# Optimization experiments

Measured on AMD Instinct MI355X. Metric: run time of the kernel, lower is better.

Reference implementation:

```python
import jax, jax.numpy as jnp
import numpy as np

K0 = 0.7978845608028654  # sqrt(2/pi)
C1 = 0.044715

def _gelu_tanh(x):
    # tanh-approx GELU, matching the Triton kernel's math
    return 0.5 * x * (1.0 + jnp.tanh(K0 * (x + C1 * x * x * x)))

def setup_inputs() -> dict:
    key = jax.random.key(0)
    k1, k2, k3 = jax.random.split(key, 3)
    B, C_in, H, W = 32, 64, 128, 128
    C_out, KH = 128, 3
    x = jax.random.normal(k1, (B, C_in, H, W), dtype=jnp.float32)
    weight = jax.random.normal(k2, (C_out, C_in, KH, KH), dtype=jnp.float32)
    bias = jax.random.normal(k3, (C_out,), dtype=jnp.float32)
    return {"x": x, "weight": weight, "bias": bias}

def reference(x, weight, bias):
    # Valid conv2d, stride 1 (NCHW, OIHW)
    y = jax.lax.conv_general_dilated(
        x, weight,
        window_strides=(1, 1), padding="VALID",
        dimension_numbers=("NCHW", "OIHW", "NCHW"))
    y = y + bias[None, :, None, None]
    y = _gelu_tanh(y)
    # global average pool over spatial dims -> [B, C_out]
    return jnp.mean(y, axis=(2, 3))
```

## Files before the change

kernel.cpp:

```cpp
#include <hip/hip_runtime.h>
#include <cstdint>
#include <cstddef>

#define GK0 0.7978845608028654f
#define GC1 0.044715f

typedef __attribute__((ext_vector_type(8))) short short8;
typedef __attribute__((ext_vector_type(4))) float floatx4;

__device__ __forceinline__ unsigned short f2bf(float f) {
  union { float f; unsigned int u; } v; v.f = f;
  unsigned int r = v.u + 0x7fffu + ((v.u >> 16) & 1u);
  return (unsigned short)(r >> 16);
}

__device__ __forceinline__ void gl_lds16(const unsigned short* g, unsigned short* l) {
  __builtin_amdgcn_global_load_lds(
      (const __attribute__((address_space(1))) unsigned int*)g,
      (__attribute__((address_space(3))) unsigned int*)l, 16, 0, 0);
}

__global__ void k_wt(const float* __restrict__ w, unsigned short* __restrict__ wt,
                     float* __restrict__ out) {
  if (blockIdx.x == 0) {
    for (int i = threadIdx.x; i < 32 * 128; i += 256) out[i] = 0.0f;
  }
  int t = blockIdx.x * 256 + threadIdx.x;
  if (t >= 128 * 64 * 9) return;
  int co = t / 576; int r = t - co * 576; int ci = r / 9; int khw = r - ci * 9;
  wt[(khw * 128 + co) * 64 + ci] = f2bf(w[t]);
}

__global__ __launch_bounds__(256, 2) void k_conv(
    const float* __restrict__ x, const unsigned short* __restrict__ wt,
    const float* __restrict__ bias, float* __restrict__ out) {
  __shared__ __align__(16) unsigned short Bs[4 * 72 * 64];
  __shared__ __align__(16) unsigned short As[4][4096];
  const int tid = threadIdx.x, lane = tid & 63, wv = tid >> 6;
  const int w0 = blockIdx.x * 64, h0 = blockIdx.y * 2, b = blockIdx.z;
  const int wm = wv & 1, wn = wv >> 1;
  const int m = lane & 15, q = lane >> 4;
  unsigned short* Asw = As[wv];

  const int srcswz = (lane >> 3) * 64 + (((lane & 7) ^ (lane >> 3)) << 3);
  auto stageA = [&](int khw) {
    const unsigned short* src = wt + khw * 8192 + wm * 4096 + srcswz;
#pragma unroll
    for (int c = 0; c < 8; c++) gl_lds16(src + c * 512, Asw + c * 512);
  };

  floatx4 acc[4][4];
#pragma unroll
  for (int i = 0; i < 4; i++)
#pragma unroll
    for (int j = 0; j < 4; j++) acc[i][j] = (floatx4){0.f, 0.f, 0.f, 0.f};

  stageA(0);

  const float* xb0 = x + (size_t)b * 64 * 16384 + (size_t)h0 * 128;
#pragma unroll
  for (int t3 = 0; t3 < 3; t3++) {
    float4 u[6];
#pragma unroll
    for (int j = 0; j < 6; j++) {
      const int v = (t3 * 6 + j) * 256 + tid;
      const int r = v / 1152, rem = v - r * 1152;
      const int ci = rem / 18, i = rem - ci * 18;
      const int wc = min(w0 + 4 * i, 124);
      u[j] = *(const float4*)(xb0 + (size_t)ci * 16384 + r * 128 + wc);
    }
#pragma unroll
    for (int j = 0; j < 6; j++) {
      const int v = (t3 * 6 + j) * 256 + tid;
      const int r = v / 1152, rem = v - r * 1152;
      const int ci = rem / 18, i = rem - ci * 18;
      unsigned short* brow = Bs + r * 4608;
      union { float4 v4; float f[4]; } w4; w4.v4 = u[j];
#pragma unroll
      for (int k2 = 0; k2 < 4; k2++) {
        const int p = 4 * i + k2;
        brow[p * 64 + (ci ^ ((p & 7) << 3))] = f2bf(w4.f[k2]);
      }
    }
  }
  __syncthreads();
#pragma unroll
  for (int kh = 0; kh < 3; kh++)
#pragma unroll
    for (int kw = 0; kw < 3; kw++) {
      const int khw = kh * 3 + kw;
      const unsigned short* bcur = Bs + (wn + kh) * 4608;
      short8 a[2][4], bf[2][4];
#pragma unroll
      for (int half = 0; half < 2; half++) {
        const int colb = half * 32 + q * 8;
#pragma unroll
        for (int mt = 0; mt < 4; mt++)
          a[half][mt] =
              *(const short8*)(Asw + (mt * 16 + m) * 64 + (colb ^ ((m & 7) << 3)));
#pragma unroll
        for (int nt = 0; nt < 4; nt++)
          bf[half][nt] = *(const short8*)(bcur + (nt * 16 + m + kw) * 64 +
                                          (colb ^ (((m + kw) & 7) << 3)));
      }
      asm volatile("s_waitcnt lgkmcnt(0)" ::: "memory");
      if (khw < 8) stageA(khw + 1);
#pragma unroll
      for (int half = 0; half < 2; half++)
#pragma unroll
        for (int mt = 0; mt < 4; mt++)
#pragma unroll
          for (int nt = 0; nt < 4; nt++)
            acc[mt][nt] = __builtin_amdgcn_mfma_f32_16x16x32_bf16(
                a[half][mt], bf[half][nt], acc[mt][nt], 0, 0, 0);
      if (khw < 8)
        asm volatile("s_waitcnt vmcnt(0)" ::: "memory");
    }

  const float inv_area = 1.0f / (126.0f * 126.0f);
  float* orow = out + b * 128;
#pragma unroll
  for (int mt = 0; mt < 4; mt++)
#pragma unroll
    for (int r2 = 0; r2 < 4; r2++) {
      const int co = wm * 64 + mt * 16 + q * 4 + r2;
      const float bv = bias[co];
      float s = 0.f;
#pragma unroll
      for (int nt = 0; nt < 4; nt++) {
        float y = acc[mt][nt][r2] + bv;
        float u = GK0 * (y + GC1 * y * y * y);
        float e = __expf(-2.0f * u);
        float g = y * __builtin_amdgcn_rcpf(1.0f + e);
        if (w0 + nt * 16 + m < 126) s += g;
      }
#pragma unroll
      for (int d = 1; d < 16; d <<= 1) s += __shfl_xor(s, d, 64);
      if (m == 0) atomicAdd(&orow[co], s * inv_area);
    }
}

extern "C" void kernel_launch(void* const* d_in, const int* in_sizes, int n_in,
                              void* d_out, int out_size, void* d_ws, size_t ws_size,
                              hipStream_t stream) {
  const float* x    = (const float*)d_in[0];
  const float* w    = (const float*)d_in[1];
  const float* bias = (const float*)d_in[2];
  float* out = (float*)d_out;

  unsigned short* wbuf = (unsigned short*)d_ws;
  if (ws_size < (size_t)9 * 128 * 64 * 2 + 4096) return;

  k_wt<<<288, 256, 0, stream>>>(w, wbuf, out);
  k_conv<<<dim3(2, 63, 32), 256, 0, stream>>>(x, wbuf, bias, out);
}
```

Before: 369.4 us.

## Make conv blocks persistent over row pairs with rolling input ring buffer

Each block now processes up to 8 output row pairs instead of one, keeping a 4-row circular LDS buffer of bf16 input rows and prefetching the next two rows into registers during the MFMA loop. Weight tiles are restaged cyclically per tap, and GELU pooling is accumulated in registers per row pair, so there are fewer atomics and input rows are reused between adjacent pairs. The grid shrinks from 63 to 8 row groups, which cuts launch parallelism to 512 blocks and adds extra syncs and register pressure from the prefetch buffers.

```diff
diff --git a/kernel.cpp b/kernel.cpp
--- a/kernel.cpp
+++ b/kernel.cpp
@@ -34,10 +34,11 @@
 __global__ __launch_bounds__(256, 2) void k_conv(
     const float* __restrict__ x, const unsigned short* __restrict__ wt,
     const float* __restrict__ bias, float* __restrict__ out) {
-  __shared__ __align__(16) unsigned short Bs[4 * 72 * 64];
+  __shared__ __align__(16) unsigned short Bs[4][4608];
   __shared__ __align__(16) unsigned short As[4][4096];
   const int tid = threadIdx.x, lane = tid & 63, wv = tid >> 6;
-  const int w0 = blockIdx.x * 64, h0 = blockIdx.y * 2, b = blockIdx.z;
+  const int w0 = blockIdx.x * 64, g = blockIdx.y, b = blockIdx.z;
+  const int npair = (g < 7) ? 8 : 7;
   const int wm = wv & 1, wn = wv >> 1;
   const int m = lane & 15, q = lane >> 4;
   unsigned short* Asw = As[wv];
@@ -49,73 +50,143 @@
     for (int c = 0; c < 8; c++) gl_lds16(src + c * 512, Asw + c * 512);
   };
 
+  const float* xg = x + (size_t)b * 64 * 16384 + (size_t)(16 * g) * 128;
+
+  float bvv[4][4];
+#pragma unroll
+  for (int mt = 0; mt < 4; mt++)
+#pragma unroll
+    for (int r2 = 0; r2 < 4; r2++)
+      bvv[mt][r2] = bias[wm * 64 + mt * 16 + q * 4 + r2];
+
   floatx4 acc[4][4];
+  float pool[4][4];
 #pragma unroll
   for (int i = 0; i < 4; i++)
 #pragma unroll
-    for (int j = 0; j < 4; j++) acc[i][j] = (floatx4){0.f, 0.f, 0.f, 0.f};
+    for (int j = 0; j < 4; j++) {
+      acc[i][j] = (floatx4){0.f, 0.f, 0.f, 0.f};
+      pool[i][j] = 0.f;
+    }
 
   stageA(0);
 
-  const float* xb0 = x + (size_t)b * 64 * 16384 + (size_t)h0 * 128;
 #pragma unroll
   for (int t3 = 0; t3 < 3; t3++) {
-    float4 u[6];
+    float4 u6[6];
 #pragma unroll
     for (int j = 0; j < 6; j++) {
-      const int v = (t3 * 6 + j) * 256 + tid;
-      const int r = v / 1152, rem = v - r * 1152;
-      const int ci = rem / 18, i = rem - ci * 18;
-      const int wc = min(w0 + 4 * i, 124);
-      u[j] = *(const float4*)(xb0 + (size_t)ci * 16384 + r * 128 + wc);
+      const int u = (t3 * 6 + j) * 256 + tid;
+      const int r = u / 1152, rem = u - r * 1152;
+      const int ci = rem / 18, ch = rem - ci * 18;
+      u6[j] = *(const float4*)(xg + (size_t)ci * 16384 + r * 128 + min(w0 + 4 * ch, 124));
     }
 #pragma unroll
     for (int j = 0; j < 6; j++) {
-      const int v = (t3 * 6 + j) * 256 + tid;
-      const int r = v / 1152, rem = v - r * 1152;
-      const int ci = rem / 18, i = rem - ci * 18;
-      unsigned short* brow = Bs + r * 4608;
-      union { float4 v4; float f[4]; } w4; w4.v4 = u[j];
-#pragma unroll
-      for (int k2 = 0; k2 < 4; k2++) {
-        const int p = 4 * i + k2;
-        brow[p * 64 + (ci ^ ((p & 7) << 3))] = f2bf(w4.f[k2]);
+      const int u = (t3 * 6 + j) * 256 + tid;
+      const int r = u / 1152, rem = u - r * 1152;
+      const int ci = rem / 18, ch = rem - ci * 18;
+      union { float4 v4; float f[4]; } fu; fu.v4 = u6[j];
+#pragma unroll
+      for (int e = 0; e < 4; e++) {
+        const int p = 4 * ch + e;
+        Bs[r][p * 64 + (ci ^ ((p & 7) << 3))] = f2bf(fu.f[e]);
       }
     }
   }
   __syncthreads();
-#pragma unroll
-  for (int kh = 0; kh < 3; kh++)
-#pragma unroll
-    for (int kw = 0; kw < 3; kw++) {
-      const int khw = kh * 3 + kw;
-      const unsigned short* bcur = Bs + (wn + kh) * 4608;
-      short8 a[2][4], bf[2][4];
-#pragma unroll
-      for (int half = 0; half < 2; half++) {
-        const int colb = half * 32 + q * 8;
-#pragma unroll
-        for (int mt = 0; mt < 4; mt++)
-          a[half][mt] =
-              *(const short8*)(Asw + (mt * 16 + m) * 64 + (colb ^ ((m & 7) << 3)));
-#pragma unroll
-        for (int nt = 0; nt < 4; nt++)
-          bf[half][nt] = *(const short8*)(bcur + (nt * 16 + m + kw) * 64 +
-                                          (colb ^ (((m + kw) & 7) << 3)));
-      }
-      asm volatile("s_waitcnt lgkmcnt(0)" ::: "memory");
-      if (khw < 8) stageA(khw + 1);
-#pragma unroll
-      for (int half = 0; half < 2; half++)
-#pragma unroll
-        for (int mt = 0; mt < 4; mt++)
+
+  for (int hp = 0; hp < npair; hp++) {
+    const int more = (hp + 1 < npair);
+    float4 ru[9];
+    unsigned int pk[9][2];
+#pragma unroll
+    for (int kh = 0; kh < 3; kh++) {
+#pragma unroll
+      for (int kw = 0; kw < 3; kw++) {
+        const int khw = kh * 3 + kw;
+        const unsigned short* bcur = Bs[(2 * hp + wn + kh) & 3];
+        short8 a[2][4], bf[2][4];
+#pragma unroll
+        for (int half = 0; half < 2; half++) {
+          const int colb = half * 32 + q * 8;
+#pragma unroll
+          for (int mt = 0; mt < 4; mt++)
+            a[half][mt] =
+                *(const short8*)(Asw + (mt * 16 + m) * 64 + (colb ^ ((m & 7) << 3)));
 #pragma unroll
           for (int nt = 0; nt < 4; nt++)
-            acc[mt][nt] = __builtin_amdgcn_mfma_f32_16x16x32_bf16(
-                a[half][mt], bf[half][nt], acc[mt][nt], 0, 0, 0);
-      if (khw < 8)
+            bf[half][nt] = *(const short8*)(bcur + (nt * 16 + m + kw) * 64 +
+                                            (colb ^ (((m + kw) & 7) << 3)));
+        }
+        asm volatile("s_waitcnt lgkmcnt(0)" ::: "memory");
+        if (!(hp == npair - 1 && khw == 8))
+          stageA((khw + 1) % 9);
+#pragma unroll
+        for (int half = 0; half < 2; half++)
+#pragma unroll
+          for (int mt = 0; mt < 4; mt++)
+#pragma unroll
+            for (int nt = 0; nt < 4; nt++)
+              acc[mt][nt] = __builtin_amdgcn_mfma_f32_16x16x32_bf16(
+                  a[half][mt], bf[half][nt], acc[mt][nt], 0, 0, 0);
         asm volatile("s_waitcnt vmcnt(0)" ::: "memory");
-    }
+        if (khw == 0 && more) {
+#pragma unroll
+          for (int k = 0; k < 9; k++) {
+            const int u = k * 256 + tid;
+            const int r2 = u / 1152, rem = u - r2 * 1152;
+            const int ci = rem / 18, ch = rem - ci * 18;
+            ru[k] = *(const float4*)(xg + (size_t)ci * 16384 +
+                                     (2 * hp + 4 + r2) * 128 + min(w0 + 4 * ch, 124));
+          }
+        }
+        if (khw == 5 && more) {
+#pragma unroll
+          for (int k = 0; k < 9; k++) {
+            union { float4 v4; float f[4]; } fu; fu.v4 = ru[k];
+            pk[k][0] = (unsigned)f2bf(fu.f[0]) | ((unsigned)f2bf(fu.f[1]) << 16);
+            pk[k][1] = (unsigned)f2bf(fu.f[2]) | ((unsigned)f2bf(fu.f[3]) << 16);
+          }
+        }
+      }
+      if (kh == 1) {
+        __syncthreads();
+        if (more) {
+#pragma unroll
+          for (int k = 0; k < 9; k++) {
+            const int u = k * 256 + tid;
+            const int rw = u / 1152, rem = u - rw * 1152;
+            const int ci = rem / 18, ch = rem - ci * 18;
+            unsigned short* dst = Bs[(2 * hp + rw) & 3];
+#pragma unroll
+            for (int e = 0; e < 4; e++) {
+              const int p = 4 * ch + e;
+              dst[p * 64 + (ci ^ ((p & 7) << 3))] =
+                  (unsigned short)((pk[k][e >> 1] >> ((e & 1) * 16)) & 0xffffu);
+            }
+          }
+        }
+      }
+    }
+#pragma unroll
+    for (int mt = 0; mt < 4; mt++)
+#pragma unroll
+      for (int r2 = 0; r2 < 4; r2++) {
+        float s = 0.f;
+#pragma unroll
+        for (int nt = 0; nt < 4; nt++) {
+          float y = acc[mt][nt][r2] + bvv[mt][r2];
+          float u = GK0 * (y + GC1 * y * y * y);
+          float e = __expf(-2.0f * u);
+          float gl = y * __builtin_amdgcn_rcpf(1.0f + e);
+          if (w0 + nt * 16 + m < 126) s += gl;
+          acc[mt][nt][r2] = 0.f;
+        }
+        pool[mt][r2] += s;
+      }
+    __syncthreads();
+  }
 
   const float inv_area = 1.0f / (126.0f * 126.0f);
   float* orow = out + b * 128;
@@ -123,20 +194,10 @@
   for (int mt = 0; mt < 4; mt++)
 #pragma unroll
     for (int r2 = 0; r2 < 4; r2++) {
-      const int co = wm * 64 + mt * 16 + q * 4 + r2;
-      const float bv = bias[co];
-      float s = 0.f;
-#pragma unroll
-      for (int nt = 0; nt < 4; nt++) {
-        float y = acc[mt][nt][r2] + bv;
-        float u = GK0 * (y + GC1 * y * y * y);
-        float e = __expf(-2.0f * u);
-        float g = y * __builtin_amdgcn_rcpf(1.0f + e);
-        if (w0 + nt * 16 + m < 126) s += g;
-      }
+      float s = pool[mt][r2];
 #pragma unroll
       for (int d = 1; d < 16; d <<= 1) s += __shfl_xor(s, d, 64);
-      if (m == 0) atomicAdd(&orow[co], s * inv_area);
+      if (m == 0) atomicAdd(&orow[wm * 64 + mt * 16 + q * 4 + r2], s * inv_area);
     }
 }
 
@@ -152,5 +213,5 @@
   if (ws_size < (size_t)9 * 128 * 64 * 2 + 4096) return;
 
   k_wt<<<288, 256, 0, stream>>>(w, wbuf, out);
-  k_conv<<<dim3(2, 63, 32), 256, 0, stream>>>(x, wbuf, bias, out);
-}
+  k_conv<<<dim3(2, 8, 32), 256, 0, stream>>>(x, wbuf, bias, out);
+}
```

Measured after the change: 528.7 us. 43.1% more time.

## Stream input rows through a two-row LDS ring to raise occupancy

Applied to the files above, without the earlier changes.

The input tile buffer in LDS shrinks from four rows to a two-row ring, and the third and fourth rows are loaded into registers during the kh loop and written into the freed slot between kh iterations. The lower LDS footprint allows launch bounds to go from 2 to 3 blocks per CU, for more latency hiding. In exchange it adds two block-wide barriers per row step and extra register pressure from the in-flight loads. It also overlaps part of the global load latency with MFMA work.

```diff
diff --git a/kernel.cpp b/kernel.cpp
--- a/kernel.cpp
+++ b/kernel.cpp
@@ -31,10 +31,10 @@
   wt[(khw * 128 + co) * 64 + ci] = f2bf(w[t]);
 }
 
-__global__ __launch_bounds__(256, 2) void k_conv(
+__global__ __launch_bounds__(256, 3) void k_conv(
     const float* __restrict__ x, const unsigned short* __restrict__ wt,
     const float* __restrict__ bias, float* __restrict__ out) {
-  __shared__ __align__(16) unsigned short Bs[4 * 72 * 64];
+  __shared__ __align__(16) unsigned short Bs[2][4608];
   __shared__ __align__(16) unsigned short As[4][4096];
   const int tid = threadIdx.x, lane = tid & 63, wv = tid >> 6;
   const int w0 = blockIdx.x * 64, h0 = blockIdx.y * 2, b = blockIdx.z;
@@ -49,47 +49,49 @@
     for (int c = 0; c < 8; c++) gl_lds16(src + c * 512, Asw + c * 512);
   };
 
+  const float* xb0 = x + (size_t)b * 64 * 16384;
+
+  stageA(0);
+
+  {
+    float4 pu[9];
+#pragma unroll
+    for (int k = 0; k < 9; k++) {
+      const int u = k * 256 + tid;
+      const int r = u / 1152, rem = u - r * 1152;
+      const int ci = rem / 18, ch = rem - ci * 18;
+      pu[k] = *(const float4*)(xb0 + (size_t)ci * 16384 + (h0 + r) * 128 +
+                               min(w0 + 4 * ch, 124));
+    }
+#pragma unroll
+    for (int k = 0; k < 9; k++) {
+      const int u = k * 256 + tid;
+      const int r = u / 1152, rem = u - r * 1152;
+      const int ci = rem / 18, ch = rem - ci * 18;
+      union { float4 v4; float f[4]; } fu; fu.v4 = pu[k];
+#pragma unroll
+      for (int e = 0; e < 4; e++) {
+        const int p = 4 * ch + e;
+        Bs[r][p * 64 + (ci ^ ((p & 7) << 3))] = f2bf(fu.f[e]);
+      }
+    }
+  }
+
   floatx4 acc[4][4];
 #pragma unroll
   for (int i = 0; i < 4; i++)
 #pragma unroll
     for (int j = 0; j < 4; j++) acc[i][j] = (floatx4){0.f, 0.f, 0.f, 0.f};
 
-  stageA(0);
+  __syncthreads();
 
-  const float* xb0 = x + (size_t)b * 64 * 16384 + (size_t)h0 * 128;
+  float4 nu[5];
 #pragma unroll
-  for (int t3 = 0; t3 < 3; t3++) {
-    float4 u[6];
-#pragma unroll
-    for (int j = 0; j < 6; j++) {
-      const int v = (t3 * 6 + j) * 256 + tid;
-      const int r = v / 1152, rem = v - r * 1152;
-      const int ci = rem / 18, i = rem - ci * 18;
-      const int wc = min(w0 + 4 * i, 124);
-      u[j] = *(const float4*)(xb0 + (size_t)ci * 16384 + r * 128 + wc);
-    }
-#pragma unroll
-    for (int j = 0; j < 6; j++) {
-      const int v = (t3 * 6 + j) * 256 + tid;
-      const int r = v / 1152, rem = v - r * 1152;
-      const int ci = rem / 18, i = rem - ci * 18;
-      unsigned short* brow = Bs + r * 4608;
-      union { float4 v4; float f[4]; } w4; w4.v4 = u[j];
-#pragma unroll
-      for (int k2 = 0; k2 < 4; k2++) {
-        const int p = 4 * i + k2;
-        brow[p * 64 + (ci ^ ((p & 7) << 3))] = f2bf(w4.f[k2]);
-      }
-    }
-  }
-  __syncthreads();
-#pragma unroll
-  for (int kh = 0; kh < 3; kh++)
+  for (int kh = 0; kh < 3; kh++) {
 #pragma unroll
     for (int kw = 0; kw < 3; kw++) {
-      const int khw = kh * 3 + kw;
-      const unsigned short* bcur = Bs + (wn + kh) * 4608;
+      const int t = kh * 3 + kw;
+      const unsigned short* bcur = Bs[(wn + kh) & 1];
       short8 a[2][4], bf[2][4];
 #pragma unroll
       for (int half = 0; half < 2; half++) {
@@ -104,7 +106,18 @@
                                           (colb ^ (((m + kw) & 7) << 3)));
       }
       asm volatile("s_waitcnt lgkmcnt(0)" ::: "memory");
-      if (khw < 8) stageA(khw + 1);
+      if (kw == 0 && kh < 2) {
+#pragma unroll
+        for (int k = 0; k < 5; k++) {
+          const int u = k * 256 + tid;
+          if (u < 1152) {
+            const int ci = u / 18, ch = u - ci * 18;
+            nu[k] = *(const float4*)(xb0 + (size_t)ci * 16384 + (h0 + kh + 2) * 128 +
+                                     min(w0 + 4 * ch, 124));
+          }
+        }
+      }
+      if (t < 8) stageA(t + 1);
 #pragma unroll
       for (int half = 0; half < 2; half++)
 #pragma unroll
@@ -113,9 +126,26 @@
           for (int nt = 0; nt < 4; nt++)
             acc[mt][nt] = __builtin_amdgcn_mfma_f32_16x16x32_bf16(
                 a[half][mt], bf[half][nt], acc[mt][nt], 0, 0, 0);
-      if (khw < 8)
-        asm volatile("s_waitcnt vmcnt(0)" ::: "memory");
+      asm volatile("s_waitcnt vmcnt(0)" ::: "memory");
     }
+    if (kh < 2) {
+      __syncthreads();
+#pragma unroll
+      for (int k = 0; k < 5; k++) {
+        const int u = k * 256 + tid;
+        if (u < 1152) {
+          const int ci = u / 18, ch = u - ci * 18;
+          union { float4 v4; float f[4]; } fu; fu.v4 = nu[k];
+#pragma unroll
+          for (int e = 0; e < 4; e++) {
+            const int p = 4 * ch + e;
+            Bs[kh & 1][p * 64 + (ci ^ ((p & 7) << 3))] = f2bf(fu.f[e]);
+          }
+        }
+      }
+      __syncthreads();
+    }
+  }
 
   const float inv_area = 1.0f / (126.0f * 126.0f);
   float* orow = out + b * 128;
```

New measurement: 372.3 us. About the same (+0.8%).
